# Kernel tuning notes

Measured on AMD Instinct MI355X. Metric: run time of the kernel, lower is better.

The kernel has to match this reference:

```python
import jax, jax.numpy as jnp
import numpy as np

D_MODEL = 1024
N_HEADS = 16
D_K = D_MODEL // N_HEADS
THETA = 10000.0
BATCH, SEQ = 4, 2048


def apply_rope(x, pos, theta=THETA):
    # x: [B, H, S, d_k]; pos: [S] int. Rotate interleaved pairs (x_{2i}, x_{2i+1}).
    half = x.shape[-1] // 2
    inv_freq = theta ** (-jnp.arange(half, dtype=x.dtype) * 2.0 / x.shape[-1])  # [half]
    ang = pos.astype(x.dtype)[:, None] * inv_freq[None, :]                      # [S, half]
    cos, sin = jnp.cos(ang), jnp.sin(ang)
    x1, x2 = x[..., 0::2], x[..., 1::2]
    r1 = x1 * cos - x2 * sin
    r2 = x1 * sin + x2 * cos
    return jnp.stack([r1, r2], axis=-1).reshape(x.shape)


def setup_inputs() -> dict:
    key = jax.random.key(0)
    k1, k2, k3 = jax.random.split(key, 3)
    x = jax.random.normal(k1, (BATCH, SEQ, D_MODEL), dtype=jnp.float32)
    W_qkv = jax.random.normal(k2, (3 * D_MODEL, D_MODEL), dtype=jnp.float32) * (D_MODEL ** -0.5)
    b_qkv = jnp.zeros((3 * D_MODEL,), dtype=jnp.float32)
    W_o = jax.random.normal(k3, (D_MODEL, D_MODEL), dtype=jnp.float32) * (D_MODEL ** -0.5)
    b_o = jnp.zeros((D_MODEL,), dtype=jnp.float32)
    token_positions = jnp.arange(SEQ, dtype=jnp.int64 if jax.config.jax_enable_x64 else jnp.int32)
    return {"x": x, "token_positions": token_positions, "W_qkv": W_qkv,
            "b_qkv": b_qkv, "W_o": W_o, "b_o": b_o}


def reference(x, token_positions, W_qkv, b_qkv, W_o, b_o):
    B, S, _ = x.shape
    qkv = x @ W_qkv.T + b_qkv                                   # [B, S, 3*d_model]
    qkv = qkv.reshape(B, S, 3, N_HEADS, D_K)
    qkv = jnp.transpose(qkv, (2, 0, 3, 1, 4))                   # [3, B, H, S, d_k]
    q, k, v = qkv[0], qkv[1], qkv[2]
    q = apply_rope(q, token_positions)
    k = apply_rope(k, token_positions)
    scores = jnp.einsum('bhqd,bhkd->bhqk', q / jnp.sqrt(jnp.asarray(D_K, x.dtype)), k)
    causal = jnp.tril(jnp.ones((S, S), dtype=bool))             # True where attended
    scores = jnp.where(causal, scores, jnp.asarray(-jnp.inf, scores.dtype))
    attn = jax.nn.softmax(scores, axis=-1)
    out = jnp.einsum('bhqk,bhkd->bhqd', attn, v)                # [B, H, S, d_k]
    out = jnp.transpose(out, (0, 2, 1, 3)).reshape(B, S, D_MODEL)
    return out @ W_o.T + b_o
```

## Files before the change

kernel.cpp:

```cpp
#include <hip/hip_runtime.h>
#include <hip/hip_bf16.h>
#include <cstdint>

#define S_LEN 2048
#define NHEAD 16
#define DMODEL 1024

using short8 = __attribute__((ext_vector_type(8))) short;
using f32x4  = __attribute__((ext_vector_type(4))) float;

__device__ __forceinline__ float bf2f(ushort u) {
    return __uint_as_float(((uint32_t)u) << 16);
}
__device__ __forceinline__ ushort f2bf(float f) {
    uint32_t u = __float_as_uint(f);
    u += 0x7FFF + ((u >> 16) & 1);
    return (ushort)(u >> 16);
}
__device__ __forceinline__ uint32_t cvt_pk_bf16(float lo, float hi) {
    uint32_t r;
    asm("v_cvt_pk_bf16_f32 %0, %1, %2" : "=v"(r) : "v"(lo), "v"(hi));
    return r;
}
__device__ __forceinline__ float exp2_(float x) {
    float r; asm("v_exp_f32 %0, %1" : "=v"(r) : "v"(x)); return r;
}
__device__ __forceinline__ float fract_(float x) {
    float r; asm("v_fract_f32 %0, %1" : "=v"(r) : "v"(x)); return r;
}
__device__ __forceinline__ float sin_rev(float x) {
    float r; asm("v_sin_f32 %0, %1" : "=v"(r) : "v"(x)); return r;
}
__device__ __forceinline__ float cos_rev(float x) {
    float r; asm("v_cos_f32 %0, %1" : "=v"(r) : "v"(x)); return r;
}
template<int N> __device__ __forceinline__ void vwait() {
    asm volatile("s_waitcnt vmcnt(%0)" :: "n"(N) : "memory");
}

__global__ void k_cast3(const float* __restrict__ x, const float* __restrict__ wqkv,
                        const float* __restrict__ wo, ushort* __restrict__ xb,
                        ushort* __restrict__ wqb, ushort* __restrict__ wob)
{
    int i = blockIdx.x * blockDim.x + threadIdx.x;
    const float* in; ushort* out; int j;
    if (i < 2097152)      { in = x;    out = xb;  j = i; }
    else if (i < 2883584) { in = wqkv; out = wqb; j = i - 2097152; }
    else                  { in = wo;   out = wob; j = i - 2883584; }
    const float4 v = reinterpret_cast<const float4*>(in)[j];
    ushort4 o;
    o.x = f2bf(v.x); o.y = f2bf(v.y); o.z = f2bf(v.z); o.w = f2bf(v.w);
    reinterpret_cast<ushort4*>(out)[j] = o;
}

__device__ __forceinline__ void gl16(const ushort* g, ushort* l) {
    __builtin_amdgcn_global_load_lds(
        (const __attribute__((address_space(1))) void*)g,
        (__attribute__((address_space(3))) void*)l, 16, 0, 0);
}

__global__ __launch_bounds__(512, 2)
void k_gemm256(const ushort* __restrict__ A, const ushort* __restrict__ Bm,
               const float* __restrict__ bias, const int* __restrict__ pos,
               ushort* __restrict__ Qo, ushort* __restrict__ Ko,
               ushort* __restrict__ Vt, int K, int nbn)
{
    __shared__ ushort As[2][16384];
    __shared__ ushort Bs[2][16384];

    const int bid = blockIdx.x;
    const int cpx = gridDim.x >> 3;
    const int wg = (bid & 7) * cpx + (bid >> 3);
    const int bn = (wg % nbn) * 256, bm = (wg / nbn) * 256;
    const int t = threadIdx.x, w = t >> 6, l = t & 63;
    const int wr = w >> 2, wc = w & 3;
    const int lr = l & 15, lg = l >> 4;

    f32x4 acc[8][4] = {};

    auto stage_pair = [&](int kt, int b, int u0) {
        #pragma unroll
        for (int uu = 0; uu < 2; ++uu) {
            const int u = u0 + uu;
            const int e = (u & 3) * 4096 + t * 8;
            const int r = e >> 6;
            const int c = (e & 63) ^ ((r & 7) << 3);
            if (u < 4) gl16(Bm + (size_t)(bn + r) * K + kt * 64 + c, &Bs[b][e]);
            else       gl16(A  + (size_t)(bm + r) * K + kt * 64 + c, &As[b][e]);
        }
    };

    const int NT = K >> 6;

    stage_pair(0, 0, 0); stage_pair(0, 0, 2);
    stage_pair(0, 0, 4); stage_pair(0, 0, 6);
    if (NT > 1) {
        stage_pair(1, 1, 0); stage_pair(1, 1, 2);
        vwait<4>();
    } else {
        vwait<0>();
    }
    __builtin_amdgcn_s_barrier();

    short8 bfr[4][2];

    for (int tt = 0; tt < NT; ++tt) {
        const int b = tt & 1;
        const ushort* Al = As[b];
        const ushort* Bl = Bs[b];

        #pragma unroll
        for (int p = 0; p < 4; ++p) {
            if (p == 0) {
                #pragma unroll
                for (int n = 0; n < 4; ++n) {
                    const int rB = wc * 64 + n * 16 + lr;
                    #pragma unroll
                    for (int kk = 0; kk < 2; ++kk)
                        bfr[n][kk] = *(const short8*)&Bl[rB * 64 + ((kk * 32 + lg * 8) ^ ((rB & 7) << 3))];
                }
            }
            short8 afr[2][2];
            #pragma unroll
            for (int jj = 0; jj < 2; ++jj) {
                const int rA = wr * 16 + 32 * (2 * p + jj) + lr;
                #pragma unroll
                for (int kk = 0; kk < 2; ++kk)
                    afr[jj][kk] = *(const short8*)&Al[rA * 64 + ((kk * 32 + lg * 8) ^ ((rA & 7) << 3))];
            }
            if      (p == 0) { if (tt + 1 < NT) stage_pair(tt + 1, b ^ 1, 4); }
            else if (p == 1) { if (tt + 1 < NT) stage_pair(tt + 1, b ^ 1, 6); }
            else if (p == 2) { if (tt + 2 < NT) stage_pair(tt + 2, b, 0); }
            else             { if (tt + 2 < NT) stage_pair(tt + 2, b, 2); }

            __builtin_amdgcn_s_barrier();
            __builtin_amdgcn_s_setprio(1);
            #pragma unroll
            for (int jj = 0; jj < 2; ++jj)
                #pragma unroll
                for (int n = 0; n < 4; ++n)
                    #pragma unroll
                    for (int kk = 0; kk < 2; ++kk)
                        acc[2 * p + jj][n] = __builtin_amdgcn_mfma_f32_16x16x32_bf16(
                            afr[jj][kk], bfr[n][kk], acc[2 * p + jj][n], 0, 0, 0);
            __builtin_amdgcn_s_setprio(0);
            if (p == 3) {
                if      (tt + 2 < NT) vwait<4>();
                else if (tt + 1 < NT) vwait<0>();
            }
            __builtin_amdgcn_s_barrier();
        }
    }

    const int col0 = bn + wc * 64 + lr;
    float bv[4];
    #pragma unroll
    for (int n = 0; n < 4; ++n) bv[n] = bias[col0 + n * 16];

    const int typ = bn >> 10;
    if (typ < 2) {
        ushort* Out = (typ == 0) ? Qo : Ko;
        const float scl = (typ == 0) ? 0.18033688f : 1.0f;
        const int h = ((bn & 1023) >> 6) + wc;
        float invf_rev[4];
        #pragma unroll
        for (int n = 0; n < 4; ++n)
            invf_rev[n] = exp2_(-(float)(n * 8 + (lr >> 1)) * 0.41524101186092f) * 0.15915494309f;
        #pragma unroll
        for (int j = 0; j < 8; ++j) {
            const int row0 = bm + wr * 16 + 32 * j + lg * 4;
            #pragma unroll
            for (int r = 0; r < 4; ++r) {
                const int row = row0 + r;
                const int s = row & 2047;
                const float p = (float)pos[s];
                const size_t obase = ((size_t)((row >> 11) * NHEAD + h) * S_LEN + s) * 64;
                #pragma unroll
                for (int n = 0; n < 4; ++n) {
                    const float v = acc[j][n][r] + bv[n];
                    const float prt = __shfl_xor(v, 1);
                    const float a = fract_(p * invf_rev[n]);
                    const float sA = sin_rev(a), cA = cos_rev(a);
                    const float res = (lr & 1) ? (prt * sA + v * cA)
                                               : (v * cA - prt * sA);
                    Out[obase + n * 16 + lr] = f2bf(res * scl);
                }
            }
        }
    } else {
        ushort* hb = (wc == 0) ? As[0] : (wc == 1) ? As[1] : (wc == 2) ? Bs[0] : Bs[1];
        #pragma unroll
        for (int j = 0; j < 8; ++j) {
            const int s = wr * 16 + 32 * j + lg * 4;
            #pragma unroll
            for (int n = 0; n < 4; ++n) {
                const int d = n * 16 + lr;
                ushort4 ov;
                #pragma unroll
                for (int r = 0; r < 4; ++r) ((ushort*)&ov)[r] = f2bf(acc[j][n][r] + bv[n]);
                const int off = (d * 512 + s * 2) ^ ((d & 7) << 3);
                *(ushort4*)((char*)hb + off) = ov;
            }
        }
        __syncthreads();
        const int b0h = (bm >> 11) * NHEAD + ((bn & 1023) >> 6);
        const int s_blk = bm & 2047;
        #pragma unroll
        for (int i = 0; i < 8; ++i) {
            const int c = i * 512 + t;
            const int hs = c >> 10, rem = c & 1023;
            const int d = rem >> 4, sc = rem & 15;
            const ushort* rb = (hs == 0) ? As[0] : (hs == 1) ? As[1] : (hs == 2) ? Bs[0] : Bs[1];
            uint2 u[4];
            #pragma unroll
            for (int q = 0; q < 4; ++q) {
                const int off = (d * 512 + sc * 32 + q * 8) ^ ((d & 7) << 3);
                u[q] = *(const uint2*)((const char*)rb + off);
            }
            ushort* dst = Vt + ((size_t)(b0h + hs) * 64 + d) * 2048 + s_blk + sc * 16;
            *(uint4*)dst = make_uint4(u[0].x, u[0].y, u[1].x, u[1].y);
            *(uint4*)(dst + 8) = make_uint4(u[2].x, u[2].y, u[3].x, u[3].y);
        }
    }
}

__global__ __launch_bounds__(256, 2)
void k_gemm_bt(const ushort* __restrict__ A, const ushort* __restrict__ Bm,
               const float* __restrict__ bias, float* __restrict__ Cout,
               int M, int N, int K, int nbn)
{
    __shared__ ushort As[128 * 32];
    __shared__ ushort Bs[128 * 32];
    const int t = threadIdx.x;
    const int w = t >> 6, l = t & 63;
    const int lr = l & 15, lg = l >> 4;
    const int bid = blockIdx.x;
    const int cpx = gridDim.x >> 3;
    const int wg = (bid & 7) * cpx + (bid >> 3);
    const int bm = (wg / nbn) * 128, bn = (wg % nbn) * 128;
    const int wr = (w >> 1) * 64, wc = (w & 1) * 64;

    f32x4 acc[4][4] = {};

    const ushort* ag = A + (size_t)(bm + (t >> 2)) * K + (t & 3) * 8;
    const ushort* bg = Bm + (size_t)(bn + (t >> 2)) * K + (t & 3) * 8;
    ushort* asd = &As[t * 8];
    ushort* bsd = &Bs[t * 8];
    const size_t rowskip = (size_t)64 * K;

    for (int k0 = 0; k0 < K; k0 += 32) {
        gl16(ag + k0, asd);
        gl16(ag + rowskip + k0, asd + 2048);
        gl16(bg + k0, bsd);
        gl16(bg + rowskip + k0, bsd + 2048);
        __syncthreads();
        short8 af[4], bf[4];
        #pragma unroll
        for (int m = 0; m < 4; ++m)
            af[m] = *reinterpret_cast<const short8*>(&As[(wr + m * 16 + lr) * 32 + lg * 8]);
        #pragma unroll
        for (int n = 0; n < 4; ++n)
            bf[n] = *reinterpret_cast<const short8*>(&Bs[(wc + n * 16 + lr) * 32 + lg * 8]);
        #pragma unroll
        for (int m = 0; m < 4; ++m)
            #pragma unroll
            for (int n = 0; n < 4; ++n)
                acc[m][n] = __builtin_amdgcn_mfma_f32_16x16x32_bf16(af[m], bf[n], acc[m][n], 0, 0, 0);
        __syncthreads();
    }

    const int col0 = bn + wc + lr;
    float bv[4];
    #pragma unroll
    for (int n = 0; n < 4; ++n) bv[n] = bias[col0 + n * 16];
    #pragma unroll
    for (int m = 0; m < 4; ++m) {
        const int row0 = bm + wr + m * 16 + lg * 4;
        #pragma unroll
        for (int r = 0; r < 4; ++r) {
            const size_t ro = (size_t)(row0 + r) * N;
            #pragma unroll
            for (int n = 0; n < 4; ++n)
                Cout[ro + col0 + n * 16] = acc[m][n][r] + bv[n];
        }
    }
}

__global__ __launch_bounds__(256, 3)
void k_attn(const ushort* __restrict__ Q, const ushort* __restrict__ Kk,
            const ushort* __restrict__ Vt, ushort* __restrict__ O)
{
    __shared__ ushort Ks[2][4096];
    __shared__ ushort Vs[2][4096];
    __shared__ ushort P[4][32][72];

    const int blk = blockIdx.x;
    const int qb = 15 - (blk >> 6);
    const int bh = blk & 63;
    const int b = bh >> 4, h = bh & 15;
    const int t = threadIdx.x, w = t >> 6, l = t & 63;
    const int lr = l & 15, lg = l >> 4;

    const ushort* Kb = Kk + (size_t)bh * S_LEN * 64;
    const ushort* Vb = Vt + (size_t)bh * 64 * S_LEN;
    const ushort* Qb = Q + (size_t)bh * S_LEN * 64;

    const int qbase0 = qb * 128 + w * 16;
    const int qbase1 = qbase0 + 64;

    short8 qf[2][2];
    #pragma unroll
    for (int qg = 0; qg < 2; ++qg)
        #pragma unroll
        for (int dh = 0; dh < 2; ++dh)
            qf[qg][dh] = *(const short8*)(Qb + (size_t)(qbase0 + qg * 64 + lr) * 64 + dh * 32 + lg * 8);

    f32x4 acc[2][4] = {};
    float ls[2] = {0.f, 0.f};
    const float M0 = 10.0f;

    const int nt = 2 * qb + 2;

    auto stage = [&](int kb2, int buf) {
        ushort* Kd = Ks[buf]; ushort* Vd = Vs[buf];
        #pragma unroll
        for (int j = 0; j < 2; ++j) {
            const int e = (j * 256 + t) * 8;
            const int row = e >> 6;
            const int col = (e & 63) ^ ((row & 7) << 3);
            gl16(Kb + (size_t)(kb2 + row) * 64 + col, Kd + e);
            gl16(Vb + (size_t)row * S_LEN + kb2 + col, Vd + e);
        }
    };

    stage(0, 0);
    __syncthreads();

    for (int kt = 0; kt < nt; ++kt) {
        const int cur = kt & 1;
        const int kb = kt * 64;
        if (kt + 1 < nt) stage(kb + 64, cur ^ 1);

        const ushort* Kl = Ks[cur];
        short8 kf[4][2];
        #pragma unroll
        for (int i = 0; i < 4; ++i) {
            const int krow = i * 16 + lr, sw = (krow & 7) << 3;
            kf[i][0] = *(const short8*)&Kl[krow * 64 + ((lg * 8) ^ sw)];
            kf[i][1] = *(const short8*)&Kl[krow * 64 + ((32 + lg * 8) ^ sw)];
        }

        auto do_group = [&](int qg, int qbaseg, bool domask) {
            f32x4 st[4] = {};
            __builtin_amdgcn_s_setprio(1);
            #pragma unroll
            for (int i = 0; i < 4; ++i) {
                st[i] = __builtin_amdgcn_mfma_f32_16x16x32_bf16(kf[i][0], qf[qg][0], st[i], 0, 0, 0);
                st[i] = __builtin_amdgcn_mfma_f32_16x16x32_bf16(kf[i][1], qf[qg][1], st[i], 0, 0, 0);
            }
            __builtin_amdgcn_s_setprio(0);
            if (domask) {
                const int qrow = qbaseg + lr;
                #pragma unroll
                for (int i = 0; i < 4; ++i)
                    #pragma unroll
                    for (int r = 0; r < 4; ++r)
                        if (kb + i * 16 + lg * 4 + r > qrow) st[i][r] = -INFINITY;
            }
            float ps = 0.f;
            #pragma unroll
            for (int i = 0; i < 4; ++i) {
                const float e0 = exp2_(st[i][0] - M0);
                const float e1 = exp2_(st[i][1] - M0);
                const float e2 = exp2_(st[i][2] - M0);
                const float e3 = exp2_(st[i][3] - M0);
                ps += (e0 + e1) + (e2 + e3);
                uint2 pk;
                pk.x = cvt_pk_bf16(e0, e1);
                pk.y = cvt_pk_bf16(e2, e3);
                *(uint2*)&P[w][qg * 16 + lr][i * 16 + lg * 4] = pk;
            }
            ps += __shfl_xor(ps, 16);
            ps += __shfl_xor(ps, 32);
            ls[qg] += ps;
        };

        const bool g0 = (kt < nt - 1);
        do_group(1, qbase1, kt == nt - 1);
        if (g0) do_group(0, qbase0, kt == nt - 2);

        short8 pf1[2], pf0[2];
        pf1[0] = *(const short8*)&P[w][16 + lr][lg * 8];
        pf1[1] = *(const short8*)&P[w][16 + lr][32 + lg * 8];
        if (g0) {
            pf0[0] = *(const short8*)&P[w][lr][lg * 8];
            pf0[1] = *(const short8*)&P[w][lr][32 + lg * 8];
        }
        const ushort* Vl = Vs[cur];
        __builtin_amdgcn_s_setprio(1);
        #pragma unroll
        for (int d = 0; d < 4; ++d) {
            const int vrow = d * 16 + lr, sw = (vrow & 7) << 3;
            short8 v0 = *(const short8*)&Vl[vrow * 64 + ((lg * 8) ^ sw)];
            short8 v1 = *(const short8*)&Vl[vrow * 64 + ((32 + lg * 8) ^ sw)];
            acc[1][d] = __builtin_amdgcn_mfma_f32_16x16x32_bf16(v0, pf1[0], acc[1][d], 0, 0, 0);
            acc[1][d] = __builtin_amdgcn_mfma_f32_16x16x32_bf16(v1, pf1[1], acc[1][d], 0, 0, 0);
            if (g0) {
                acc[0][d] = __builtin_amdgcn_mfma_f32_16x16x32_bf16(v0, pf0[0], acc[0][d], 0, 0, 0);
                acc[0][d] = __builtin_amdgcn_mfma_f32_16x16x32_bf16(v1, pf0[1], acc[0][d], 0, 0, 0);
            }
        }
        __builtin_amdgcn_s_setprio(0);
        __syncthreads();
    }

    #pragma unroll
    for (int qg = 0; qg < 2; ++qg) {
        const float inv = 1.f / ls[qg];
        const int q = qbase0 + qg * 64 + lr;
        #pragma unroll
        for (int d = 0; d < 4; ++d) {
            ushort4 ov;
            #pragma unroll
            for (int r = 0; r < 4; ++r) ((ushort*)&ov)[r] = f2bf(acc[qg][d][r] * inv);
            *(ushort4*)&O[((size_t)(b * S_LEN) + q) * 1024 + h * 64 + d * 16 + lg * 4] = ov;
        }
    }
}

extern "C" void kernel_launch(void* const* d_in, const int* in_sizes, int n_in,
                              void* d_out, int out_size, void* d_ws, size_t ws_size,
                              hipStream_t stream)
{
    const float* x    = (const float*)d_in[0];
    const int*   pos  = (const int*)d_in[1];
    const float* Wqkv = (const float*)d_in[2];
    const float* bqkv = (const float*)d_in[3];
    const float* Wo   = (const float*)d_in[4];
    const float* bo   = (const float*)d_in[5];
    float* out = (float*)d_out;

    char* ws = (char*)d_ws;
    ushort* xb   = (ushort*)(ws);
    ushort* wqb  = (ushort*)(ws + 16777216);
    ushort* wob  = (ushort*)(ws + 23068672);
    ushort* Qb   = (ushort*)(ws + 75497472);
    ushort* Kb   = (ushort*)(ws + 92274688);
    ushort* Vtb  = (ushort*)(ws + 109051904);
    ushort* AOb  = (ushort*)(ws + 125829120);

    k_cast3<<<12288, 256, 0, stream>>>(x, Wqkv, Wo, xb, wqb, wob);
    k_gemm256<<<384, 512, 0, stream>>>(xb, wqb, bqkv, pos, Qb, Kb, Vtb, 1024, 12);
    k_attn<<<1024, 256, 0, stream>>>(Qb, Kb, Vtb, AOb);
    k_gemm_bt<<<512, 256, 0, stream>>>(AOb, wob, bo, out, 8192, 1024, 1024, 8);
}
```

Measured before the change: 164.2 us.

## Halve QKV GEMM K-tile to raise occupancy, restage LDS pipeline and V transpose

The 256x256 QKV GEMM now uses a K-tile of 32 instead of 64, which halves LDS per block (64KB) and raises the launch-bounds occupancy target from 2 to 4 blocks per CU. The swizzle, staging schedule and MFMA loop are restructured for the narrower tile, with two half-step compute phases per K iteration. The V transpose epilogue is split into two passes so it fits in the smaller shared buffers. The aim is better latency hiding through more resident waves, at the cost of twice as many barriers per unit of K and tighter register limits that may cause spills with a 128-float accumulator.

```diff
diff --git a/kernel.cpp b/kernel.cpp
--- a/kernel.cpp
+++ b/kernel.cpp
@@ -59,14 +59,14 @@
         (__attribute__((address_space(3))) void*)l, 16, 0, 0);
 }
 
-__global__ __launch_bounds__(512, 2)
+__global__ __launch_bounds__(512, 4)
 void k_gemm256(const ushort* __restrict__ A, const ushort* __restrict__ Bm,
                const float* __restrict__ bias, const int* __restrict__ pos,
                ushort* __restrict__ Qo, ushort* __restrict__ Ko,
                ushort* __restrict__ Vt, int K, int nbn)
 {
-    __shared__ ushort As[2][16384];
-    __shared__ ushort Bs[2][16384];
+    __shared__ ushort As[2][8192];
+    __shared__ ushort Bs[2][8192];
 
     const int bid = blockIdx.x;
     const int cpx = gridDim.x >> 3;
@@ -78,78 +78,69 @@
 
     f32x4 acc[8][4] = {};
 
-    auto stage_pair = [&](int kt, int b, int u0) {
-        #pragma unroll
-        for (int uu = 0; uu < 2; ++uu) {
-            const int u = u0 + uu;
-            const int e = (u & 3) * 4096 + t * 8;
-            const int r = e >> 6;
-            const int c = (e & 63) ^ ((r & 7) << 3);
-            if (u < 4) gl16(Bm + (size_t)(bn + r) * K + kt * 64 + c, &Bs[b][e]);
-            else       gl16(A  + (size_t)(bm + r) * K + kt * 64 + c, &As[b][e]);
-        }
+    auto stageU = [&](int kt, int b, int u) {
+        const int E = (u & 1) * 4096 + t * 8;
+        const int r = E >> 5;
+        const int c = E & 31;
+        const int cs = (c & 7) | ((((c >> 3) ^ ((r >> 1) & 3)) & 3) << 3);
+        if (u < 2) gl16(A  + (size_t)(bm + r) * K + kt * 32 + cs, &As[b][E]);
+        else       gl16(Bm + (size_t)(bn + r) * K + kt * 32 + cs, &Bs[b][E]);
     };
 
-    const int NT = K >> 6;
-
-    stage_pair(0, 0, 0); stage_pair(0, 0, 2);
-    stage_pair(0, 0, 4); stage_pair(0, 0, 6);
-    if (NT > 1) {
-        stage_pair(1, 1, 0); stage_pair(1, 1, 2);
-        vwait<4>();
-    } else {
-        vwait<0>();
-    }
+    const int NT = K >> 5;
+
+    stageU(0, 0, 0); stageU(0, 0, 2); stageU(0, 0, 3);
+    stageU(0, 0, 1);
+    stageU(1, 1, 0); stageU(1, 1, 2); stageU(1, 1, 3);
+    vwait<4>();
     __builtin_amdgcn_s_barrier();
-
-    short8 bfr[4][2];
 
     for (int tt = 0; tt < NT; ++tt) {
         const int b = tt & 1;
         const ushort* Al = As[b];
         const ushort* Bl = Bs[b];
 
-        #pragma unroll
-        for (int p = 0; p < 4; ++p) {
-            if (p == 0) {
-                #pragma unroll
-                for (int n = 0; n < 4; ++n) {
-                    const int rB = wc * 64 + n * 16 + lr;
-                    #pragma unroll
-                    for (int kk = 0; kk < 2; ++kk)
-                        bfr[n][kk] = *(const short8*)&Bl[rB * 64 + ((kk * 32 + lg * 8) ^ ((rB & 7) << 3))];
-                }
-            }
-            short8 afr[2][2];
-            #pragma unroll
-            for (int jj = 0; jj < 2; ++jj) {
-                const int rA = wr * 16 + 32 * (2 * p + jj) + lr;
-                #pragma unroll
-                for (int kk = 0; kk < 2; ++kk)
-                    afr[jj][kk] = *(const short8*)&Al[rA * 64 + ((kk * 32 + lg * 8) ^ ((rA & 7) << 3))];
-            }
-            if      (p == 0) { if (tt + 1 < NT) stage_pair(tt + 1, b ^ 1, 4); }
-            else if (p == 1) { if (tt + 1 < NT) stage_pair(tt + 1, b ^ 1, 6); }
-            else if (p == 2) { if (tt + 2 < NT) stage_pair(tt + 2, b, 0); }
-            else             { if (tt + 2 < NT) stage_pair(tt + 2, b, 2); }
-
-            __builtin_amdgcn_s_barrier();
-            __builtin_amdgcn_s_setprio(1);
-            #pragma unroll
-            for (int jj = 0; jj < 2; ++jj)
-                #pragma unroll
-                for (int n = 0; n < 4; ++n)
-                    #pragma unroll
-                    for (int kk = 0; kk < 2; ++kk)
-                        acc[2 * p + jj][n] = __builtin_amdgcn_mfma_f32_16x16x32_bf16(
-                            afr[jj][kk], bfr[n][kk], acc[2 * p + jj][n], 0, 0, 0);
-            __builtin_amdgcn_s_setprio(0);
-            if (p == 3) {
-                if      (tt + 2 < NT) vwait<4>();
-                else if (tt + 1 < NT) vwait<0>();
-            }
-            __builtin_amdgcn_s_barrier();
-        }
+        short8 bfr[4], afr[4];
+        #pragma unroll
+        for (int n = 0; n < 4; ++n) {
+            const int rB = wc * 64 + n * 16 + lr;
+            bfr[n] = *(const short8*)&Bl[rB * 32 + ((lg ^ ((rB >> 1) & 3)) << 3)];
+        }
+        #pragma unroll
+        for (int j = 0; j < 4; ++j) {
+            const int rA = wr * 16 + 32 * j + lr;
+            afr[j] = *(const short8*)&Al[rA * 32 + ((lg ^ ((rA >> 1) & 3)) << 3)];
+        }
+        if (tt + 1 < NT) stageU(tt + 1, b ^ 1, 1);
+        __builtin_amdgcn_s_barrier();
+        __builtin_amdgcn_s_setprio(1);
+        #pragma unroll
+        for (int j = 0; j < 4; ++j)
+            #pragma unroll
+            for (int n = 0; n < 4; ++n)
+                acc[j][n] = __builtin_amdgcn_mfma_f32_16x16x32_bf16(afr[j], bfr[n], acc[j][n], 0, 0, 0);
+        __builtin_amdgcn_s_setprio(0);
+        if (tt + 1 < NT) vwait<4>();
+        __builtin_amdgcn_s_barrier();
+
+        short8 afr2[4];
+        #pragma unroll
+        for (int j = 0; j < 4; ++j) {
+            const int rA = wr * 16 + 32 * (4 + j) + lr;
+            afr2[j] = *(const short8*)&Al[rA * 32 + ((lg ^ ((rA >> 1) & 3)) << 3)];
+        }
+        if (tt + 2 < NT) { stageU(tt + 2, b, 0); stageU(tt + 2, b, 2); stageU(tt + 2, b, 3); }
+        __builtin_amdgcn_s_barrier();
+        __builtin_amdgcn_s_setprio(1);
+        #pragma unroll
+        for (int j = 0; j < 4; ++j)
+            #pragma unroll
+            for (int n = 0; n < 4; ++n)
+                acc[4 + j][n] = __builtin_amdgcn_mfma_f32_16x16x32_bf16(afr2[j], bfr[n], acc[4 + j][n], 0, 0, 0);
+        __builtin_amdgcn_s_setprio(0);
+        if      (tt + 2 < NT) vwait<4>();
+        else if (tt + 1 < NT) vwait<0>();
+        __builtin_amdgcn_s_barrier();
     }
 
     const int col0 = bn + wc * 64 + lr;
@@ -188,38 +179,46 @@
             }
         }
     } else {
-        ushort* hb = (wc == 0) ? As[0] : (wc == 1) ? As[1] : (wc == 2) ? Bs[0] : Bs[1];
-        #pragma unroll
-        for (int j = 0; j < 8; ++j) {
-            const int s = wr * 16 + 32 * j + lg * 4;
-            #pragma unroll
-            for (int n = 0; n < 4; ++n) {
-                const int d = n * 16 + lr;
-                ushort4 ov;
-                #pragma unroll
-                for (int r = 0; r < 4; ++r) ((ushort*)&ov)[r] = f2bf(acc[j][n][r] + bv[n]);
-                const int off = (d * 512 + s * 2) ^ ((d & 7) << 3);
-                *(ushort4*)((char*)hb + off) = ov;
-            }
-        }
-        __syncthreads();
+        ushort* R0 = (ushort*)As;
+        ushort* R1 = (ushort*)Bs;
         const int b0h = (bm >> 11) * NHEAD + ((bn & 1023) >> 6);
         const int s_blk = bm & 2047;
         #pragma unroll
-        for (int i = 0; i < 8; ++i) {
-            const int c = i * 512 + t;
-            const int hs = c >> 10, rem = c & 1023;
-            const int d = rem >> 4, sc = rem & 15;
-            const ushort* rb = (hs == 0) ? As[0] : (hs == 1) ? As[1] : (hs == 2) ? Bs[0] : Bs[1];
-            uint2 u[4];
-            #pragma unroll
-            for (int q = 0; q < 4; ++q) {
-                const int off = (d * 512 + sc * 32 + q * 8) ^ ((d & 7) << 3);
-                u[q] = *(const uint2*)((const char*)rb + off);
-            }
-            ushort* dst = Vt + ((size_t)(b0h + hs) * 64 + d) * 2048 + s_blk + sc * 16;
-            *(uint4*)dst = make_uint4(u[0].x, u[0].y, u[1].x, u[1].y);
-            *(uint4*)(dst + 8) = make_uint4(u[2].x, u[2].y, u[3].x, u[3].y);
+        for (int pass = 0; pass < 2; ++pass) {
+            if ((wc >> 1) == pass) {
+                ushort* hb = (wc & 1) ? R1 : R0;
+                #pragma unroll
+                for (int j = 0; j < 8; ++j) {
+                    const int s = wr * 16 + 32 * j + lg * 4;
+                    #pragma unroll
+                    for (int n = 0; n < 4; ++n) {
+                        const int d = n * 16 + lr;
+                        ushort4 ov;
+                        #pragma unroll
+                        for (int r = 0; r < 4; ++r) ((ushort*)&ov)[r] = f2bf(acc[j][n][r] + bv[n]);
+                        const int off = (d * 512 + s * 2) ^ ((d & 7) << 3);
+                        *(ushort4*)((char*)hb + off) = ov;
+                    }
+                }
+            }
+            __syncthreads();
+            #pragma unroll
+            for (int i = 0; i < 4; ++i) {
+                const int c = i * 512 + t;
+                const int hs = c >> 10, rem = c & 1023;
+                const int d = rem >> 4, sc = rem & 15;
+                const ushort* rb = hs ? R1 : R0;
+                uint2 u[4];
+                #pragma unroll
+                for (int q = 0; q < 4; ++q) {
+                    const int off = (d * 512 + sc * 32 + q * 8) ^ ((d & 7) << 3);
+                    u[q] = *(const uint2*)((const char*)rb + off);
+                }
+                ushort* dst = Vt + ((size_t)(b0h + pass * 2 + hs) * 64 + d) * 2048 + s_blk + sc * 16;
+                *(uint4*)dst = make_uint4(u[0].x, u[0].y, u[1].x, u[1].y);
+                *(uint4*)(dst + 8) = make_uint4(u[2].x, u[2].y, u[3].x, u[3].y);
+            }
+            __syncthreads();
         }
     }
 }
```

Result: slower. 564.6 us (+244.0%).
